# Kernel optimization log

Measured on AMD Instinct MI355X. Metric: run time of the kernel, lower is better.

The kernel has to match this reference:

```python
import jax, jax.numpy as jnp
import numpy as np

N_NODES = 100000
N_EDGES = 1600000
IN_F, HID_F, OUT_F = 128, 128, 128


def setup_inputs() -> dict:
    key = jax.random.key(0)
    k1, k2, k3, k4, k5, k6 = jax.random.split(key, 6)
    x = jax.random.normal(k1, (N_NODES, IN_F), dtype=jnp.float32)
    edge_index = jax.random.randint(k2, (2, N_EDGES), 0, N_NODES, dtype=jnp.int32)
    # nn.Linear params (PyTorch layout: W [out, in], y = x @ W.T + b)
    s1 = 1.0 / np.sqrt(IN_F)
    W1 = jax.random.uniform(k3, (HID_F, IN_F), minval=-s1, maxval=s1, dtype=jnp.float32)
    b1 = jax.random.uniform(k4, (HID_F,), minval=-s1, maxval=s1, dtype=jnp.float32)
    s2 = 1.0 / np.sqrt(HID_F)
    W2 = jax.random.uniform(k5, (OUT_F, HID_F), minval=-s2, maxval=s2, dtype=jnp.float32)
    b2 = jax.random.uniform(k6, (OUT_F,), minval=-s2, maxval=s2, dtype=jnp.float32)
    return {"x": x, "edge_index": edge_index, "W1": W1, "b1": b1, "W2": W2, "b2": b2}


def _spmm_mean(h, row, col, deg_inv):
    # (adj @ h)[i] = sum_{edges e: row[e]==i} h[col[e]], then scale by deg_inv[i]
    agg = jax.ops.segment_sum(h[col], row, num_segments=N_NODES)
    return agg * deg_inv[:, None]


def reference(x, edge_index, W1, b1, W2, b2):
    row, col = edge_index[0], edge_index[1]
    # degree = row-sum of adjacency (duplicates in COO are summed, matching torch)
    deg = jax.ops.segment_sum(jnp.ones((N_EDGES,), dtype=x.dtype), row, num_segments=N_NODES)
    deg_inv = jnp.where(deg > 0, 1.0 / deg, 0.0)
    # dropout in eval mode = identity
    h = x @ W1.T + b1
    h = _spmm_mean(h, row, col, deg_inv)
    h = jax.nn.elu(h)
    h = h @ W2.T + b2
    h = _spmm_mean(h, row, col, deg_inv)
    return h
```

## Files before the change

kernel.cpp:

```cpp
#include <hip/hip_runtime.h>
#include <math.h>

#define N_NODES 100000
#define N_EDGES 1600000
#define F 128
#define NBUCK 196
#define EPB 4096
#define CAP 9216

typedef _Float16 f16x2 __attribute__((ext_vector_type(2)));
typedef _Float16 f16x8 __attribute__((ext_vector_type(8)));
typedef __fp16 fp16x2 __attribute__((ext_vector_type(2)));
typedef float f32x2 __attribute__((ext_vector_type(2)));
typedef float f32x4 __attribute__((ext_vector_type(4)));

__device__ inline uint pkrtz(float a, float b) {
    union { fp16x2 h; uint u; } c;
    c.h = __builtin_amdgcn_cvt_pkrtz(a, b);
    return c.u;
}
__device__ inline f16x2 as2(uint u) {
    union { uint u; f16x2 h; } c; c.u = u; return c.h;
}

__device__ inline int wave_incl_scan(int v, int lane) {
#pragma unroll
    for (int off = 1; off < 64; off <<= 1) {
        int t = __shfl_up(v, off);
        if (lane >= off) v += t;
    }
    return v;
}


__global__ __launch_bounds__(512) void bucketize_kernel(const int* __restrict__ row,
                                                        const int* __restrict__ col,
                                                        int* __restrict__ bucket_cursor,
                                                        int* __restrict__ pairs) {
    __shared__ int stage[EPB];
    __shared__ unsigned char bid[EPB];
    __shared__ int lcnt[NBUCK], lcur[NBUCK], loff[NBUCK], gbase[NBUCK];
    __shared__ int wsum[8];
    const int tid = threadIdx.x;
    const int lane = tid & 63;
    const int wid = tid >> 6;
    const int base = blockIdx.x * EPB;
    const int cnt = min(N_EDGES - base, EPB);

    for (int i = tid; i < NBUCK; i += 512) { lcnt[i] = 0; lcur[i] = 0; }
    __syncthreads();
    for (int i = 0; i < EPB / 512; ++i) {
        int e = base + i * 512 + tid;
        if (e < N_EDGES) atomicAdd(&lcnt[row[e] >> 9], 1);
    }
    __syncthreads();
    {
        int v = (tid < NBUCK) ? lcnt[tid] : 0;
        int inc = wave_incl_scan(v, lane);
        if (lane == 63) wsum[wid] = inc;
        __syncthreads();
        if (tid == 0) {
            int a = 0;
#pragma unroll
            for (int i = 0; i < 8; ++i) { int t = wsum[i]; wsum[i] = a; a += t; }
        }
        __syncthreads();
        if (tid < NBUCK) loff[tid] = inc - v + wsum[wid];
    }
    if (tid < NBUCK) {
        int c = lcnt[tid];
        gbase[tid] = c ? atomicAdd(&bucket_cursor[tid], c) : 0;
    }
    __syncthreads();
    for (int i = 0; i < EPB / 512; ++i) {
        int e = base + i * 512 + tid;
        if (e < N_EDGES) {
            int r = row[e], c = col[e];
            int b = r >> 9;
            int rk = atomicAdd(&lcur[b], 1);
            int q = loff[b] + rk;
            stage[q] = ((r & 511) << 17) | c;
            bid[q] = (unsigned char)b;
        }
    }
    __syncthreads();
    for (int q = tid; q < cnt; q += 512) {
        int b = bid[q];
        int t = gbase[b] + (q - loff[b]);
        if (t < CAP) pairs[b * CAP + t] = stage[q];
    }
}

__global__ __launch_bounds__(1024) void csr_finalize_kernel(const int* __restrict__ pairs,
                                                            const int* __restrict__ bucket_cursor,
                                                            int* __restrict__ csr_col,
                                                            int2* __restrict__ rs,
                                                            float* __restrict__ deg_inv) {
    __shared__ int rcnt[512], rcnt2[512], roff[512];
    __shared__ int colstage[CAP];
    __shared__ int wsum[8];
    const int tid = threadIdx.x;
    const int lane = tid & 63;
    const int wid = tid >> 6;
    const int b = blockIdx.x;
    const int cnt = min(bucket_cursor[b], CAP);
    const int base = b * CAP;
    const int* reg = &pairs[base];

    if (tid < 512) { rcnt[tid] = 0; rcnt2[tid] = 0; }
    __syncthreads();
    for (int q = tid; q < cnt; q += 1024) atomicAdd(&rcnt[reg[q] >> 17], 1);
    __syncthreads();
    int d = 0, inc = 0;
    if (tid < 512) {
        d = rcnt[tid];
        inc = wave_incl_scan(d, lane);
        if (lane == 63) wsum[wid] = inc;
    }
    __syncthreads();
    if (tid == 0) {
        int a = 0;
#pragma unroll
        for (int i = 0; i < 8; ++i) { int t = wsum[i]; wsum[i] = a; a += t; }
    }
    __syncthreads();
    if (tid < 512) {
        const int excl = inc - d + wsum[wid];
        roff[tid] = excl;
        const int grow = (b << 9) + tid;
        if (grow < N_NODES) {
            rs[grow] = make_int2(base + excl, d);
            deg_inv[grow] = d ? 1.0f / (float)d : 0.0f;
        }
    }
    __syncthreads();
    for (int q = tid; q < cnt; q += 1024) {
        int v = reg[q];
        int lr = v >> 17;
        int rk = atomicAdd(&rcnt2[lr], 1);
        colstage[roff[lr] + rk] = v & 0x1FFFF;
    }
    __syncthreads();
    for (int q = tid; q < cnt; q += 1024) csr_col[base + q] = colstage[q];
}


#define XCHUNKS (N_NODES * F / 8 / 256)

__global__ __launch_bounds__(256) void convert_xw_kernel(const float* __restrict__ X,
                                                         const float* __restrict__ W1,
                                                         const float* __restrict__ W2,
                                                         uint* __restrict__ Xh,
                                                         uint* __restrict__ W1h,
                                                         uint* __restrict__ W2h) {
    const int b = blockIdx.x;
    if (b < XCHUNKS) {
        int i = b * 256 + threadIdx.x;
        float4 a = *(const float4*)&X[(size_t)i * 8];
        float4 c = *(const float4*)&X[(size_t)i * 8 + 4];
        uint4 o = {pkrtz(a.x, a.y), pkrtz(a.z, a.w), pkrtz(c.x, c.y), pkrtz(c.z, c.w)};
        *(uint4*)&Xh[(size_t)i * 4] = o;
    } else {
        int i = (b - XCHUNKS) * 256 + threadIdx.x;
        if (i < F * F / 2) {
            float2 a = *(const float2*)&W1[i * 2];
            float2 c = *(const float2*)&W2[i * 2];
            W1h[i] = pkrtz(a.x, a.y);
            W2h[i] = pkrtz(c.x, c.y);
        }
    }
}


template <bool ELU, bool OUT_F32>
__global__ __launch_bounds__(128, 8) void fused_agg_gemm_kernel(
        const ushort* __restrict__ H,
        const int2* __restrict__ rs,
        const int* __restrict__ csr_col,
        const float* __restrict__ deg_inv,
        const ushort* __restrict__ Wh,
        const float* __restrict__ bias,
        void* __restrict__ out) {
    __shared__ __align__(16) ushort xs[32 * 136];

    const int tid = threadIdx.x;
    const int wv = tid >> 6;
    const int lane = tid & 63;
    const int m0 = (blockIdx.x << 5) + (wv << 4);
    const int qw = lane >> 4;
    const int fo = (lane & 15) << 3;
    ushort* xw = &xs[(wv << 4) * 136];

    for (int rr = 0; rr < 4; ++rr) {
        const int rowi = qw * 4 + rr;
        const int node = m0 + rowi;
        f32x2 a[4];
#pragma unroll
        for (int i = 0; i < 4; ++i) a[i] = (f32x2){0.f, 0.f};
        const int2 sd = rs[node];
        int p = sd.x;
        const int e = sd.x + sd.y;
        const float di = deg_inv[node];
        while (p + 7 < e) {
            int cc[8];
#pragma unroll
            for (int k = 0; k < 8; ++k) cc[k] = __builtin_nontemporal_load(&csr_col[p + k]);
            uint4 vv[8];
#pragma unroll
            for (int k = 0; k < 8; ++k) vv[k] = *(const uint4*)&H[(size_t)cc[k] * F + fo];
#pragma unroll
            for (int k = 0; k < 8; k += 4) {
                f16x2 h0 = (as2(vv[k].x) + as2(vv[k + 1].x)) + (as2(vv[k + 2].x) + as2(vv[k + 3].x));
                f16x2 h1 = (as2(vv[k].y) + as2(vv[k + 1].y)) + (as2(vv[k + 2].y) + as2(vv[k + 3].y));
                f16x2 h2 = (as2(vv[k].z) + as2(vv[k + 1].z)) + (as2(vv[k + 2].z) + as2(vv[k + 3].z));
                f16x2 h3 = (as2(vv[k].w) + as2(vv[k + 1].w)) + (as2(vv[k + 2].w) + as2(vv[k + 3].w));
                a[0] += (f32x2){(float)h0.x, (float)h0.y};
                a[1] += (f32x2){(float)h1.x, (float)h1.y};
                a[2] += (f32x2){(float)h2.x, (float)h2.y};
                a[3] += (f32x2){(float)h3.x, (float)h3.y};
            }
            p += 8;
        }
        if (p + 3 < e) {
            int c0 = csr_col[p], c1 = csr_col[p + 1], c2 = csr_col[p + 2], c3 = csr_col[p + 3];
            uint4 v0 = *(const uint4*)&H[(size_t)c0 * F + fo];
            uint4 v1 = *(const uint4*)&H[(size_t)c1 * F + fo];
            uint4 v2 = *(const uint4*)&H[(size_t)c2 * F + fo];
            uint4 v3 = *(const uint4*)&H[(size_t)c3 * F + fo];
            f16x2 h0 = (as2(v0.x) + as2(v1.x)) + (as2(v2.x) + as2(v3.x));
            f16x2 h1 = (as2(v0.y) + as2(v1.y)) + (as2(v2.y) + as2(v3.y));
            f16x2 h2 = (as2(v0.z) + as2(v1.z)) + (as2(v2.z) + as2(v3.z));
            f16x2 h3 = (as2(v0.w) + as2(v1.w)) + (as2(v2.w) + as2(v3.w));
            a[0] += (f32x2){(float)h0.x, (float)h0.y};
            a[1] += (f32x2){(float)h1.x, (float)h1.y};
            a[2] += (f32x2){(float)h2.x, (float)h2.y};
            a[3] += (f32x2){(float)h3.x, (float)h3.y};
            p += 4;
        }
        if (p + 1 < e) {
            int c0 = csr_col[p], c1 = csr_col[p + 1];
            uint4 v0 = *(const uint4*)&H[(size_t)c0 * F + fo];
            uint4 v1 = *(const uint4*)&H[(size_t)c1 * F + fo];
            f16x2 h0 = as2(v0.x) + as2(v1.x);
            f16x2 h1 = as2(v0.y) + as2(v1.y);
            f16x2 h2 = as2(v0.z) + as2(v1.z);
            f16x2 h3 = as2(v0.w) + as2(v1.w);
            a[0] += (f32x2){(float)h0.x, (float)h0.y};
            a[1] += (f32x2){(float)h1.x, (float)h1.y};
            a[2] += (f32x2){(float)h2.x, (float)h2.y};
            a[3] += (f32x2){(float)h3.x, (float)h3.y};
            p += 2;
        }
        if (p < e) {
            int c = csr_col[p];
            uint4 v = *(const uint4*)&H[(size_t)c * F + fo];
            f16x2 h0 = as2(v.x), h1 = as2(v.y), h2 = as2(v.z), h3 = as2(v.w);
            a[0] += (f32x2){(float)h0.x, (float)h0.y};
            a[1] += (f32x2){(float)h1.x, (float)h1.y};
            a[2] += (f32x2){(float)h2.x, (float)h2.y};
            a[3] += (f32x2){(float)h3.x, (float)h3.y};
        }
        uint4 o = {pkrtz(a[0].x * di, a[0].y * di), pkrtz(a[1].x * di, a[1].y * di),
                   pkrtz(a[2].x * di, a[2].y * di), pkrtz(a[3].x * di, a[3].y * di)};
        *(uint4*)&xw[rowi * 136 + fo] = o;
    }

    const int q = lane >> 4;
    const int t = lane & 15;

    f16x8 xfr[4];
#pragma unroll
    for (int kk = 0; kk < 4; ++kk)
        xfr[kk] = *(const f16x8*)&xw[t * 136 + kk * 32 + q * 8];

    f32x4 acc[8];
#pragma unroll
    for (int j = 0; j < 8; ++j) acc[j] = (f32x4){0.f, 0.f, 0.f, 0.f};

#pragma unroll
    for (int j = 0; j < 8; ++j) {
        const ushort* wrow = &Wh[(j * 16 + t) * F + q * 8];
#pragma unroll
        for (int kk = 0; kk < 4; ++kk) {
            f16x8 wfr = *(const f16x8*)&wrow[kk * 32];
            acc[j] = __builtin_amdgcn_mfma_f32_16x16x32_f16(wfr, xfr[kk], acc[j], 0, 0, 0);
        }
    }

    const int node = m0 + t;
    const float dv = deg_inv[node];
    const float mk = (dv > 0.f) ? 1.f : 0.f;

#pragma unroll
    for (int j = 0; j < 8; ++j) {
        f32x4 bb = *(const f32x4*)&bias[j * 16 + q * 4];
        f32x4 v = acc[j] + bb * mk;
        if (ELU) {
#pragma unroll
            for (int r = 0; r < 4; ++r) v[r] = (v[r] > 0.f) ? v[r] : expm1f(v[r]);
        }
        if (OUT_F32) {
            float* of = &((float*)out)[(size_t)node * F + j * 16 + q * 4];
            __builtin_nontemporal_store(v, (f32x4*)of);
        } else {
            uint2 o = {pkrtz(v[0], v[1]), pkrtz(v[2], v[3])};
            *(uint2*)&((ushort*)out)[(size_t)node * F + j * 16 + q * 4] = o;
        }
    }
}


extern "C" void kernel_launch(void* const* d_in, const int* in_sizes, int n_in,
                              void* d_out, int out_size, void* d_ws, size_t ws_size,
                              hipStream_t stream) {
    const float* x  = (const float*)d_in[0];
    const int*   ei = (const int*)d_in[1];
    const float* W1 = (const float*)d_in[2];
    const float* b1 = (const float*)d_in[3];
    const float* W2 = (const float*)d_in[4];
    const float* b2 = (const float*)d_in[5];
    float* out = (float*)d_out;

    const int* row = ei;
    const int* col = ei + N_EDGES;

    ushort* bufA = (ushort*)d_ws;
    ushort* bufB = bufA + (size_t)N_NODES * F;
    int* csr_col = (int*)(bufB + (size_t)N_NODES * F);
    int2* rs = (int2*)(csr_col + NBUCK * CAP);
    float* deg_inv = (float*)(rs + N_NODES + 4);
    int* bucket_cursor = (int*)(deg_inv + N_NODES);
    uint* W1h = (uint*)(bucket_cursor + 256);
    uint* W2h = W1h + F * F / 2;
    int* pairs = (int*)bufA;

    (void)hipMemsetAsync(bucket_cursor, 0, NBUCK * sizeof(int), stream);
    bucketize_kernel<<<(N_EDGES + EPB - 1) / EPB, 512, 0, stream>>>(row, col, bucket_cursor, pairs);
    csr_finalize_kernel<<<NBUCK, 1024, 0, stream>>>(pairs, bucket_cursor, csr_col, rs, deg_inv);

    convert_xw_kernel<<<XCHUNKS + 32, 256, 0, stream>>>(x, W1, W2, (uint*)bufB, W1h, W2h);

    const int fb = N_NODES / 32;
    fused_agg_gemm_kernel<true, false><<<fb, 128, 0, stream>>>(
        (const ushort*)bufB, rs, csr_col, deg_inv, (const ushort*)W1h, b1, bufA);
    fused_agg_gemm_kernel<false, true><<<fb, 128, 0, stream>>>(
        bufA, rs, csr_col, deg_inv, (const ushort*)W2h, b2, out);
}
```

Baseline: 307.0 us.

## Assign one node per 16-thread group and split GEMM output columns across waves

The fused aggregate+GEMM kernel now uses 256-thread blocks covering 16 nodes. Each 16-lane group gathers one node's neighbours, where before each group looped over four nodes serially. After a block barrier, each of the four waves computes two of the eight 16-column output tiles. This exposes more independent gathers per node and shrinks the accumulator register footprint to raise memory-level parallelism, at the cost of a __syncthreads and the B fragments being loaded redundantly across waves.

```diff
diff --git a/kernel.cpp b/kernel.cpp
--- a/kernel.cpp
+++ b/kernel.cpp
@@ -173,7 +173,7 @@
 
 
 template <bool ELU, bool OUT_F32>
-__global__ __launch_bounds__(128, 8) void fused_agg_gemm_kernel(
+__global__ __launch_bounds__(256, 6) void fused_agg_gemm_kernel(
         const ushort* __restrict__ H,
         const int2* __restrict__ rs,
         const int* __restrict__ csr_col,
@@ -181,19 +181,15 @@
         const ushort* __restrict__ Wh,
         const float* __restrict__ bias,
         void* __restrict__ out) {
-    __shared__ __align__(16) ushort xs[32 * 136];
+    __shared__ __align__(16) ushort xs[16 * 136];
 
     const int tid = threadIdx.x;
-    const int wv = tid >> 6;
-    const int lane = tid & 63;
-    const int m0 = (blockIdx.x << 5) + (wv << 4);
-    const int qw = lane >> 4;
-    const int fo = (lane & 15) << 3;
-    ushort* xw = &xs[(wv << 4) * 136];
-
-    for (int rr = 0; rr < 4; ++rr) {
-        const int rowi = qw * 4 + rr;
-        const int node = m0 + rowi;
+    const int m0 = blockIdx.x << 4;
+    const int g = tid >> 4;
+    const int fo = (tid & 15) << 3;
+
+    {
+        const int node = m0 + g;
         f32x2 a[4];
 #pragma unroll
         for (int i = 0; i < 4; ++i) a[i] = (f32x2){0.f, 0.f};
@@ -262,39 +258,36 @@
         }
         uint4 o = {pkrtz(a[0].x * di, a[0].y * di), pkrtz(a[1].x * di, a[1].y * di),
                    pkrtz(a[2].x * di, a[2].y * di), pkrtz(a[3].x * di, a[3].y * di)};
-        *(uint4*)&xw[rowi * 136 + fo] = o;
-    }
-
+        *(uint4*)&xs[g * 136 + fo] = o;
+    }
+    __syncthreads();
+
+    const int w = tid >> 6;
+    const int lane = tid & 63;
     const int q = lane >> 4;
     const int t = lane & 15;
 
     f16x8 xfr[4];
 #pragma unroll
     for (int kk = 0; kk < 4; ++kk)
-        xfr[kk] = *(const f16x8*)&xw[t * 136 + kk * 32 + q * 8];
-
-    f32x4 acc[8];
-#pragma unroll
-    for (int j = 0; j < 8; ++j) acc[j] = (f32x4){0.f, 0.f, 0.f, 0.f};
-
-#pragma unroll
-    for (int j = 0; j < 8; ++j) {
-        const ushort* wrow = &Wh[(j * 16 + t) * F + q * 8];
-#pragma unroll
-        for (int kk = 0; kk < 4; ++kk) {
-            f16x8 wfr = *(const f16x8*)&wrow[kk * 32];
-            acc[j] = __builtin_amdgcn_mfma_f32_16x16x32_f16(wfr, xfr[kk], acc[j], 0, 0, 0);
-        }
-    }
+        xfr[kk] = *(const f16x8*)&xs[t * 136 + kk * 32 + q * 8];
 
     const int node = m0 + t;
     const float dv = deg_inv[node];
     const float mk = (dv > 0.f) ? 1.f : 0.f;
 
 #pragma unroll
-    for (int j = 0; j < 8; ++j) {
+    for (int jj = 0; jj < 2; ++jj) {
+        const int j = (w << 1) | jj;
+        f32x4 acc = (f32x4){0.f, 0.f, 0.f, 0.f};
+        const ushort* wrow = &Wh[(j * 16 + t) * F + q * 8];
+#pragma unroll
+        for (int kk = 0; kk < 4; ++kk) {
+            f16x8 wfr = *(const f16x8*)&wrow[kk * 32];
+            acc = __builtin_amdgcn_mfma_f32_16x16x32_f16(wfr, xfr[kk], acc, 0, 0, 0);
+        }
         f32x4 bb = *(const f32x4*)&bias[j * 16 + q * 4];
-        f32x4 v = acc[j] + bb * mk;
+        f32x4 v = acc + bb * mk;
         if (ELU) {
 #pragma unroll
             for (int r = 0; r < 4; ++r) v[r] = (v[r] > 0.f) ? v[r] : expm1f(v[r]);
@@ -340,9 +333,9 @@
 
     convert_xw_kernel<<<XCHUNKS + 32, 256, 0, stream>>>(x, W1, W2, (uint*)bufB, W1h, W2h);
 
-    const int fb = N_NODES / 32;
-    fused_agg_gemm_kernel<true, false><<<fb, 128, 0, stream>>>(
+    const int fb = N_NODES / 16;
+    fused_agg_gemm_kernel<true, false><<<fb, 256, 0, stream>>>(
         (const ushort*)bufB, rs, csr_col, deg_inv, (const ushort*)W1h, b1, bufA);
-    fused_agg_gemm_kernel<false, true><<<fb, 128, 0, stream>>>(
+    fused_agg_gemm_kernel<false, true><<<fb, 256, 0, stream>>>(
         bufA, rs, csr_col, deg_inv, (const ushort*)W2h, b2, out);
 }
```

Result: faster. 283.8 us (-7.6%).
